# Performance work log

Measured on AMD Instinct MI355X. Metric: run time of the kernel, lower is better.

## Reference

```python
import jax, jax.numpy as jnp
import numpy as np

BATCH = 16384
MAX_ACTIVE = 32
FEAT = 768
HIDDEN = 1024


def setup_inputs() -> dict:
    key = jax.random.key(0)
    k1, k2, k3, k4, k5, k6 = jax.random.split(key, 6)
    stm = jax.random.randint(k1, (BATCH, MAX_ACTIVE), 0, FEAT, dtype=jnp.int32)
    nstm = jax.random.randint(k2, (BATCH, MAX_ACTIVE), 0, FEAT, dtype=jnp.int32)
    # Linear params (PyTorch layout: weight is (out_features, in_features))
    ft_w = jax.random.normal(k3, (HIDDEN, FEAT), dtype=jnp.float32) * 0.05
    ft_b = jax.random.normal(k4, (HIDDEN,), dtype=jnp.float32) * 0.05
    out_w = jax.random.normal(k5, (1, 2 * HIDDEN), dtype=jnp.float32) * 0.05
    out_b = jax.random.normal(k6, (1,), dtype=jnp.float32) * 0.05
    return {"stm": stm, "nstm": nstm, "ft_w": ft_w, "ft_b": ft_b,
            "out_w": out_w, "out_b": out_b}


def sparse_to_dense(indices: jnp.ndarray, size: int = FEAT) -> jnp.ndarray:
    """(B, max_active) int indices with -1 padding -> (B, size) 0/1 float32."""
    b = indices.shape[0]
    valid = (indices >= 0).astype(jnp.float32)          # (B, A)
    cols = jnp.clip(indices, 0, size - 1)               # padded -> col 0, masked by `valid`
    rows = jnp.arange(b, dtype=jnp.int32)[:, None]      # (B, 1) broadcast
    dense = jnp.zeros((b, size), dtype=jnp.float32)
    # .max matches torch's set-to-1 semantics even if duplicate indices occur
    return dense.at[rows, cols].max(valid)


def reference(stm, nstm, ft_w, ft_b, out_w, out_b):
    stm_d = sparse_to_dense(stm)                        # (B, 768)
    nstm_d = sparse_to_dense(nstm)                      # (B, 768)
    stm_h = stm_d @ ft_w.T + ft_b                       # (B, H)
    nstm_h = nstm_d @ ft_w.T + ft_b                     # (B, H)
    hidden = jnp.concatenate([stm_h, nstm_h], axis=1)   # (B, 2H)
    hidden = jnp.clip(hidden, 0.0, 1.0)
    return jax.nn.sigmoid(hidden @ out_w.T + out_b)     # (B, 1)
```

## Files before the change

### kernel.cpp

```cpp
#include <hip/hip_runtime.h>
#include <stdint.h>

#define BATCH 16384
#define MAXA 32
#define FEAT 768
#define HIDDEN 1024

#define KC 24
#define NT 32
#define ASTRIDE 784
#define AWBYTES (32 * ASTRIDE)
#define BTILE (KC * 1024)

typedef int v4i  __attribute__((ext_vector_type(4)));
typedef int v16i __attribute__((ext_vector_type(16)));

__global__ __launch_bounds__(256) void prep_quant(const float* __restrict__ ftw,
                                                  uint8_t* __restrict__ Bf,
                                                  float* __restrict__ scale,
                                                  float* __restrict__ outz) {
  const int h0 = blockIdx.x * 8;
  const int hloc = threadIdx.x >> 5;
  const int l32 = threadIdx.x & 31;
  const int h = h0 + hloc;

  float w[24];
  float amax = 0.f;
  const float* __restrict__ src = ftw + (size_t)h * FEAT;
#pragma unroll
  for (int k = 0; k < 24; ++k) {
    w[k] = src[l32 + 32 * k];
    amax = fmaxf(amax, fabsf(w[k]));
  }
#pragma unroll
  for (int m = 1; m <= 16; m <<= 1)
    amax = fmaxf(amax, __shfl_xor(amax, m, 64));
  amax = fmaxf(amax, 1e-20f);
  if (l32 == 0) scale[h] = amax / 127.f;
  const float inv = 127.f / amax;

  __shared__ __align__(16) uint8_t tile[8][ASTRIDE];
#pragma unroll
  for (int k = 0; k < 24; ++k) {
    int q = __float2int_rn(w[k] * inv);
    tile[hloc][l32 + 32 * k] = (uint8_t)(int8_t)q;
  }
  __syncthreads();

  for (int g = threadIdx.x; g < 8 * 48; g += 256) {
    int hl = g / 48, fg = g % 48;
    int kc = fg >> 1, lh = fg & 1;
    int hh = h0 + hl;
    uint4 v = *(const uint4*)&tile[hl][fg * 16];
    size_t daddr = ((size_t)((hh >> 5) * KC + kc) << 10) +
                   (size_t)(((lh << 5) | (hh & 31)) << 4);
    *(uint4*)(Bf + daddr) = v;
  }

  if (threadIdx.x < 128)
    outz[blockIdx.x * 128 + threadIdx.x] = 0.f;
}

__global__ __launch_bounds__(256, 1) void nn_mfma(
    const int* __restrict__ stm, const int* __restrict__ nstm,
    const uint8_t* __restrict__ Bf, const float* __restrict__ scale,
    const float* __restrict__ bias, const float* __restrict__ outw,
    float* __restrict__ outz)
{
  const int tid  = threadIdx.x;
  const int lane = tid & 63;
  const int wid  = tid >> 6;
  const int side = wid & 1;
  const int rgrp = wid >> 1;
  const int r0   = blockIdx.x * 64 + rgrp * 32;
  const int l31  = lane & 31;
  const int lh   = lane >> 5;

  __shared__ __align__(16) uint8_t Ash[4 * AWBYTES];
  __shared__ __align__(16) uint8_t Bbuf[2][BTILE];

  uint8_t* Aw = Ash + wid * AWBYTES;

  uint4 st[6];
  {
    const uint4* g = (const uint4*)Bf;
#pragma unroll
    for (int s = 0; s < 6; ++s) st[s] = g[s * 256 + tid];
  }

  const uint4 z4 = {0u, 0u, 0u, 0u};
#pragma unroll
  for (int it = 0; it < 25; ++it) {
    int off = it * 1024 + lane * 16;
    if (off < AWBYTES) *(uint4*)(Aw + off) = z4;
  }
  const int* __restrict__ isrc = side ? nstm : stm;
#pragma unroll
  for (int i = 0; i < 16; ++i) {
    int row = i * 2 + lh;
    int idx = isrc[(r0 + row) * MAXA + l31];
    if (idx >= 0) Aw[row * ASTRIDE + idx] = 1;
  }
  v4i areg[KC];
#pragma unroll
  for (int kc = 0; kc < KC; ++kc)
    areg[kc] = *(const v4i*)(Aw + l31 * ASTRIDE + kc * 32 + lh * 16);

#pragma unroll
  for (int s = 0; s < 6; ++s) ((uint4*)Bbuf[0])[s * 256 + tid] = st[s];
  __syncthreads();

  float* sbo = (float*)Ash;
  {
    const float4* gs = (const float4*)scale;
    const float4* gb = (const float4*)bias;
    const float4* go = (const float4*)outw;
    float4* d = (float4*)sbo;
    d[tid]       = gs[tid];
    d[256 + tid] = gb[tid];
    d[512 + tid] = go[tid];
    d[768 + tid] = go[256 + tid];
  }
  __syncthreads();

  float prow[16];
#pragma unroll
  for (int r = 0; r < 16; ++r) prow[r] = 0.f;

#pragma unroll 1
  for (int nt = 0; nt < NT; ++nt) {
    const int p = nt & 1;
    if (nt + 1 < NT) {
      const uint4* g = (const uint4*)(Bf + (size_t)(nt + 1) * BTILE);
#pragma unroll
      for (int s = 0; s < 6; ++s) st[s] = g[s * 256 + tid];
    }
    v16i acc;
#pragma unroll
    for (int r = 0; r < 16; ++r) acc[r] = 0;
    const uint8_t* bp = Bbuf[p];
#pragma unroll
    for (int kc = 0; kc < KC; ++kc) {
      v4i b = *(const v4i*)(bp + kc * 1024 + lane * 16);
      acc = __builtin_amdgcn_mfma_i32_32x32x32_i8(areg[kc], b, acc, 0, 0, 0);
    }
    float s  = sbo[nt * 32 + l31];
    float bb = sbo[1024 + nt * 32 + l31];
    float o  = sbo[2048 + side * HIDDEN + nt * 32 + l31];
#pragma unroll
    for (int r = 0; r < 16; ++r) {
      float hv = fminf(fmaxf(fmaf((float)acc[r], s, bb), 0.f), 1.f);
      prow[r] = fmaf(hv, o, prow[r]);
    }
    if (nt + 1 < NT) {
      uint4* d = (uint4*)Bbuf[p ^ 1];
#pragma unroll
      for (int s2 = 0; s2 < 6; ++s2) d[s2 * 256 + tid] = st[s2];
    }
    __syncthreads();
  }

#pragma unroll
  for (int off = 16; off >= 1; off >>= 1)
#pragma unroll
    for (int r = 0; r < 16; ++r) prow[r] += __shfl_xor(prow[r], off, 64);

  if (l31 == 0) {
#pragma unroll
    for (int r = 0; r < 16; ++r) {
      int row = (r & 3) + 8 * (r >> 2) + 4 * lh;
      atomicAdd(&outz[r0 + row], prow[r]);
    }
  }
}

__global__ __launch_bounds__(256) void nn_finish(float* __restrict__ outz,
                                                 const float* __restrict__ outb) {
  const int i = blockIdx.x * 256 + threadIdx.x;
  float y = outz[i] + outb[0];
  outz[i] = 1.f / (1.f + __expf(-y));
}

extern "C" void kernel_launch(void* const* d_in, const int* in_sizes, int n_in,
                              void* d_out, int out_size, void* d_ws, size_t ws_size,
                              hipStream_t stream) {
  const int*   stm  = (const int*)d_in[0];
  const int*   nstm = (const int*)d_in[1];
  const float* ftw  = (const float*)d_in[2];
  const float* ftb  = (const float*)d_in[3];
  const float* outw = (const float*)d_in[4];
  const float* outb = (const float*)d_in[5];

  uint8_t* Bf    = (uint8_t*)d_ws;
  float*   scale = (float*)(Bf + (size_t)FEAT * HIDDEN);
  float*   outz  = (float*)d_out;

  prep_quant<<<HIDDEN / 8, 256, 0, stream>>>(ftw, Bf, scale, outz);
  nn_mfma<<<BATCH / 64, 256, 0, stream>>>(stm, nstm, Bf, scale, ftb, outw, outz);
  nn_finish<<<BATCH / 256, 256, 0, stream>>>(outz, outb);
}
```

Measured before the change: 140.8 us.

## Process two row tiles per wave and split hidden dimension across block pairs

Each block now handles 128 batch rows instead of 64, with every wave holding two 32-row A fragments in registers, and the hidden dimension is split in half across paired blocks. Each B tile loaded into LDS therefore feeds two MFMAs, which halves B traffic per row computed while keeping the grid size the same. Register pressure roughly doubles for the A operands and accumulators, which could cause spills, and the number of atomics per output row doubles.

```diff
diff --git a/kernel.cpp b/kernel.cpp
--- a/kernel.cpp
+++ b/kernel.cpp
@@ -7,7 +7,7 @@
 #define HIDDEN 1024
 
 #define KC 24
-#define NT 32
+#define NTH 16
 #define ASTRIDE 784
 #define AWBYTES (32 * ASTRIDE)
 #define BTILE (KC * 1024)
@@ -72,7 +72,8 @@
   const int wid  = tid >> 6;
   const int side = wid & 1;
   const int rgrp = wid >> 1;
-  const int r0   = blockIdx.x * 64 + rgrp * 32;
+  const int nh   = blockIdx.x & 1;
+  const int R    = (blockIdx.x >> 1) * 128;
   const int l31  = lane & 31;
   const int lh   = lane >> 5;
 
@@ -83,28 +84,31 @@
 
   uint4 st[6];
   {
-    const uint4* g = (const uint4*)Bf;
+    const uint4* g = (const uint4*)(Bf + (size_t)(nh * NTH) * BTILE);
 #pragma unroll
     for (int s = 0; s < 6; ++s) st[s] = g[s * 256 + tid];
   }
 
+  const int* __restrict__ isrc = side ? nstm : stm;
   const uint4 z4 = {0u, 0u, 0u, 0u};
-#pragma unroll
-  for (int it = 0; it < 25; ++it) {
-    int off = it * 1024 + lane * 16;
-    if (off < AWBYTES) *(uint4*)(Aw + off) = z4;
-  }
-  const int* __restrict__ isrc = side ? nstm : stm;
-#pragma unroll
-  for (int i = 0; i < 16; ++i) {
-    int row = i * 2 + lh;
-    int idx = isrc[(r0 + row) * MAXA + l31];
-    if (idx >= 0) Aw[row * ASTRIDE + idx] = 1;
-  }
-  v4i areg[KC];
-#pragma unroll
-  for (int kc = 0; kc < KC; ++kc)
-    areg[kc] = *(const v4i*)(Aw + l31 * ASTRIDE + kc * 32 + lh * 16);
+  v4i areg[2][KC];
+#pragma unroll
+  for (int t = 0; t < 2; ++t) {
+#pragma unroll
+    for (int it = 0; it < 25; ++it) {
+      int off = it * 1024 + lane * 16;
+      if (off < AWBYTES) *(uint4*)(Aw + off) = z4;
+    }
+#pragma unroll
+    for (int i = 0; i < 16; ++i) {
+      int row = i * 2 + lh;
+      int idx = isrc[(R + rgrp * 64 + t * 32 + row) * MAXA + l31];
+      if (idx >= 0) Aw[row * ASTRIDE + idx] = 1;
+    }
+#pragma unroll
+    for (int kc = 0; kc < KC; ++kc)
+      areg[t][kc] = *(const v4i*)(Aw + l31 * ASTRIDE + kc * 32 + lh * 16);
+  }
 
 #pragma unroll
   for (int s = 0; s < 6; ++s) ((uint4*)Bbuf[0])[s * 256 + tid] = st[s];
@@ -112,47 +116,49 @@
 
   float* sbo = (float*)Ash;
   {
-    const float4* gs = (const float4*)scale;
-    const float4* gb = (const float4*)bias;
-    const float4* go = (const float4*)outw;
+    const float4* g0 = (const float4*)(scale + nh * 512);
+    const float4* g1 = (const float4*)(bias + nh * 512);
+    const float4* g2 = (const float4*)(outw + nh * 512);
+    const float4* g3 = (const float4*)(outw + HIDDEN + nh * 512);
     float4* d = (float4*)sbo;
-    d[tid]       = gs[tid];
-    d[256 + tid] = gb[tid];
-    d[512 + tid] = go[tid];
-    d[768 + tid] = go[256 + tid];
+    d[tid]       = (tid < 128) ? g0[tid] : g1[tid - 128];
+    d[256 + tid] = (tid < 128) ? g2[tid] : g3[tid - 128];
   }
   __syncthreads();
 
-  float prow[16];
-#pragma unroll
-  for (int r = 0; r < 16; ++r) prow[r] = 0.f;
+  float prow0[16], prow1[16];
+#pragma unroll
+  for (int r = 0; r < 16; ++r) { prow0[r] = 0.f; prow1[r] = 0.f; }
 
 #pragma unroll 1
-  for (int nt = 0; nt < NT; ++nt) {
+  for (int nt = 0; nt < NTH; ++nt) {
     const int p = nt & 1;
-    if (nt + 1 < NT) {
-      const uint4* g = (const uint4*)(Bf + (size_t)(nt + 1) * BTILE);
+    if (nt + 1 < NTH) {
+      const uint4* g = (const uint4*)(Bf + (size_t)(nh * NTH + nt + 1) * BTILE);
 #pragma unroll
       for (int s = 0; s < 6; ++s) st[s] = g[s * 256 + tid];
     }
-    v16i acc;
-#pragma unroll
-    for (int r = 0; r < 16; ++r) acc[r] = 0;
+    v16i acc0, acc1;
+#pragma unroll
+    for (int r = 0; r < 16; ++r) { acc0[r] = 0; acc1[r] = 0; }
     const uint8_t* bp = Bbuf[p];
 #pragma unroll
     for (int kc = 0; kc < KC; ++kc) {
       v4i b = *(const v4i*)(bp + kc * 1024 + lane * 16);
-      acc = __builtin_amdgcn_mfma_i32_32x32x32_i8(areg[kc], b, acc, 0, 0, 0);
+      acc0 = __builtin_amdgcn_mfma_i32_32x32x32_i8(areg[0][kc], b, acc0, 0, 0, 0);
+      acc1 = __builtin_amdgcn_mfma_i32_32x32x32_i8(areg[1][kc], b, acc1, 0, 0, 0);
     }
     float s  = sbo[nt * 32 + l31];
-    float bb = sbo[1024 + nt * 32 + l31];
-    float o  = sbo[2048 + side * HIDDEN + nt * 32 + l31];
+    float bb = sbo[512 + nt * 32 + l31];
+    float o  = sbo[1024 + side * 512 + nt * 32 + l31];
 #pragma unroll
     for (int r = 0; r < 16; ++r) {
-      float hv = fminf(fmaxf(fmaf((float)acc[r], s, bb), 0.f), 1.f);
-      prow[r] = fmaf(hv, o, prow[r]);
-    }
-    if (nt + 1 < NT) {
+      float h0 = fminf(fmaxf(fmaf((float)acc0[r], s, bb), 0.f), 1.f);
+      float h1 = fminf(fmaxf(fmaf((float)acc1[r], s, bb), 0.f), 1.f);
+      prow0[r] = fmaf(h0, o, prow0[r]);
+      prow1[r] = fmaf(h1, o, prow1[r]);
+    }
+    if (nt + 1 < NTH) {
       uint4* d = (uint4*)Bbuf[p ^ 1];
 #pragma unroll
       for (int s2 = 0; s2 < 6; ++s2) d[s2 * 256 + tid] = st[s2];
@@ -163,13 +169,17 @@
 #pragma unroll
   for (int off = 16; off >= 1; off >>= 1)
 #pragma unroll
-    for (int r = 0; r < 16; ++r) prow[r] += __shfl_xor(prow[r], off, 64);
+    for (int r = 0; r < 16; ++r) {
+      prow0[r] += __shfl_xor(prow0[r], off, 64);
+      prow1[r] += __shfl_xor(prow1[r], off, 64);
+    }
 
   if (l31 == 0) {
 #pragma unroll
     for (int r = 0; r < 16; ++r) {
-      int row = (r & 3) + 8 * (r >> 2) + 4 * lh;
-      atomicAdd(&outz[r0 + row], prow[r]);
+      int crow = (r & 3) + 8 * (r >> 2) + 4 * lh;
+      atomicAdd(&outz[R + rgrp * 64 + crow], prow0[r]);
+      atomicAdd(&outz[R + rgrp * 64 + 32 + crow], prow1[r]);
     }
   }
 }
@@ -196,6 +206,7 @@
   float*   outz  = (float*)d_out;
 
   prep_quant<<<HIDDEN / 8, 256, 0, stream>>>(ftw, Bf, scale, outz);
-  nn_mfma<<<BATCH / 64, 256, 0, stream>>>(stm, nstm, Bf, scale, ftb, outw, outz);
+  nn_mfma<<<(BATCH / 128) * 2, 256, 0, stream>>>(stm, nstm, Bf, scale, ftb,
+                                                 outw, outz);
   nn_finish<<<BATCH / 256, 256, 0, stream>>>(outz, outb);
 }
```

New measurement: 138.6 us. No clear change (-1.5%).

## Split hidden dim across blocks, bitmap A build, stream B directly from global

Applied to the files above, without the earlier changes.

Each block now takes 128 rows and one half of the hidden dimension (512 threads, 8 waves), so the grid doubles and each wave runs 16 N-tiles instead of 32. The dense one-hot A tile is replaced by a 32-bit-per-word bitmap in LDS built with atomicOr, then expanded to int8 bytes in registers by a multiply-and-mask trick. This shrinks LDS use enough for 2 blocks per CU. The LDS double-buffering of B is removed: waves read B fragments straight from global/L2, which drops all per-tile barriers. Two independent accumulators let consecutive MFMAs run without waiting on each other. The risk is heavier global/L2 traffic for B, since each wave re-reads it with no shared staging.

```diff
diff --git a/kernel.cpp b/kernel.cpp
--- a/kernel.cpp
+++ b/kernel.cpp
@@ -7,10 +7,9 @@
 #define HIDDEN 1024
 
 #define KC 24
-#define NT 32
+#define NTH 16
+#define BTILE (KC * 1024)
 #define ASTRIDE 784
-#define AWBYTES (32 * ASTRIDE)
-#define BTILE (KC * 1024)
 
 typedef int v4i  __attribute__((ext_vector_type(4)));
 typedef int v16i __attribute__((ext_vector_type(16)));
@@ -61,7 +60,7 @@
     outz[blockIdx.x * 128 + threadIdx.x] = 0.f;
 }
 
-__global__ __launch_bounds__(256, 1) void nn_mfma(
+__global__ __launch_bounds__(512, 2) void nn_mfma(
     const int* __restrict__ stm, const int* __restrict__ nstm,
     const uint8_t* __restrict__ Bf, const float* __restrict__ scale,
     const float* __restrict__ bias, const float* __restrict__ outw,
@@ -72,92 +71,79 @@
   const int wid  = tid >> 6;
   const int side = wid & 1;
   const int rgrp = wid >> 1;
-  const int r0   = blockIdx.x * 64 + rgrp * 32;
+  const int nh   = blockIdx.x & 1;
+  const int R    = (blockIdx.x >> 1) * 128;
   const int l31  = lane & 31;
   const int lh   = lane >> 5;
 
-  __shared__ __align__(16) uint8_t Ash[4 * AWBYTES];
-  __shared__ __align__(16) uint8_t Bbuf[2][BTILE];
+  __shared__ uint32_t amap[8][32 * 24];
+  __shared__ float    sbo[2048];
 
-  uint8_t* Aw = Ash + wid * AWBYTES;
-
-  uint4 st[6];
   {
-    const uint4* g = (const uint4*)Bf;
-#pragma unroll
-    for (int s = 0; s < 6; ++s) st[s] = g[s * 256 + tid];
+    float4* d = (float4*)sbo;
+    if (tid < 128)       d[tid] = ((const float4*)(scale + nh * 512))[tid];
+    else if (tid < 256)  d[tid] = ((const float4*)(bias + nh * 512))[tid - 128];
+    else if (tid < 384)  d[tid] = ((const float4*)(outw + nh * 512))[tid - 256];
+    else                 d[tid] = ((const float4*)(outw + HIDDEN + nh * 512))[tid - 384];
   }
 
-  const uint4 z4 = {0u, 0u, 0u, 0u};
-#pragma unroll
-  for (int it = 0; it < 25; ++it) {
-    int off = it * 1024 + lane * 16;
-    if (off < AWBYTES) *(uint4*)(Aw + off) = z4;
+  uint32_t* mp = amap[wid];
+  {
+    const uint4 z = {0u, 0u, 0u, 0u};
+    ((uint4*)mp)[lane] = z;
+    ((uint4*)mp)[64 + lane] = z;
+    ((uint4*)mp)[128 + lane] = z;
   }
   const int* __restrict__ isrc = side ? nstm : stm;
 #pragma unroll
   for (int i = 0; i < 16; ++i) {
-    int row = i * 2 + lh;
-    int idx = isrc[(r0 + row) * MAXA + l31];
-    if (idx >= 0) Aw[row * ASTRIDE + idx] = 1;
+    int row = 2 * i + lh;
+    int idx = isrc[(R + rgrp * 32 + row) * MAXA + l31];
+    if (idx >= 0) atomicOr(&mp[row * 24 + (idx >> 5)], 1u << (idx & 31));
   }
+  __syncthreads();
+
   v4i areg[KC];
 #pragma unroll
-  for (int kc = 0; kc < KC; ++kc)
-    areg[kc] = *(const v4i*)(Aw + l31 * ASTRIDE + kc * 32 + lh * 16);
-
+  for (int kc = 0; kc < KC; ++kc) {
+    uint32_t wbits = mp[l31 * 24 + kc];
+    uint32_t hbits = (wbits >> (lh * 16)) & 0xFFFFu;
+    v4i a;
 #pragma unroll
-  for (int s = 0; s < 6; ++s) ((uint4*)Bbuf[0])[s * 256 + tid] = st[s];
-  __syncthreads();
-
-  float* sbo = (float*)Ash;
-  {
-    const float4* gs = (const float4*)scale;
-    const float4* gb = (const float4*)bias;
-    const float4* go = (const float4*)outw;
-    float4* d = (float4*)sbo;
-    d[tid]       = gs[tid];
-    d[256 + tid] = gb[tid];
-    d[512 + tid] = go[tid];
-    d[768 + tid] = go[256 + tid];
+    for (int j = 0; j < 4; ++j)
+      a[j] = (int)((((hbits >> (4 * j)) & 0xFu) * 0x00204081u) & 0x01010101u);
+    areg[kc] = a;
   }
-  __syncthreads();
 
   float prow[16];
 #pragma unroll
   for (int r = 0; r < 16; ++r) prow[r] = 0.f;
 
+  const uint8_t* __restrict__ Bbase =
+      Bf + (size_t)(nh * NTH) * BTILE + (size_t)lane * 16;
+
 #pragma unroll 1
-  for (int nt = 0; nt < NT; ++nt) {
-    const int p = nt & 1;
-    if (nt + 1 < NT) {
-      const uint4* g = (const uint4*)(Bf + (size_t)(nt + 1) * BTILE);
+  for (int nt = 0; nt < NTH; ++nt) {
+    const uint8_t* bp = Bbase + (size_t)nt * BTILE;
+    v16i acc0, acc1;
 #pragma unroll
-      for (int s = 0; s < 6; ++s) st[s] = g[s * 256 + tid];
-    }
-    v16i acc;
+    for (int r = 0; r < 16; ++r) { acc0[r] = 0; acc1[r] = 0; }
 #pragma unroll
-    for (int r = 0; r < 16; ++r) acc[r] = 0;
-    const uint8_t* bp = Bbuf[p];
-#pragma unroll
-    for (int kc = 0; kc < KC; ++kc) {
-      v4i b = *(const v4i*)(bp + kc * 1024 + lane * 16);
-      acc = __builtin_amdgcn_mfma_i32_32x32x32_i8(areg[kc], b, acc, 0, 0, 0);
+    for (int kc = 0; kc < KC; kc += 2) {
+      v4i b0 = *(const v4i*)(bp + (size_t)kc * 1024);
+      v4i b1 = *(const v4i*)(bp + (size_t)kc * 1024 + 1024);
+      acc0 = __builtin_amdgcn_mfma_i32_32x32x32_i8(areg[kc], b0, acc0, 0, 0, 0);
+      acc1 = __builtin_amdgcn_mfma_i32_32x32x32_i8(areg[kc + 1], b1, acc1, 0, 0, 0);
     }
     float s  = sbo[nt * 32 + l31];
-    float bb = sbo[1024 + nt * 32 + l31];
-    float o  = sbo[2048 + side * HIDDEN + nt * 32 + l31];
+    float bb = sbo[512 + nt * 32 + l31];
+    float o  = sbo[1024 + side * 512 + nt * 32 + l31];
 #pragma unroll
     for (int r = 0; r < 16; ++r) {
-      float hv = fminf(fmaxf(fmaf((float)acc[r], s, bb), 0.f), 1.f);
+      int q = acc0[r] + acc1[r];
+      float hv = fminf(fmaxf(fmaf((float)q, s, bb), 0.f), 1.f);
       prow[r] = fmaf(hv, o, prow[r]);
     }
-    if (nt + 1 < NT) {
-      uint4* d = (uint4*)Bbuf[p ^ 1];
-#pragma unroll
-      for (int s2 = 0; s2 < 6; ++s2) d[s2 * 256 + tid] = st[s2];
-    }
-    __syncthreads();
   }
 
 #pragma unroll
@@ -168,8 +154,8 @@
   if (l31 == 0) {
 #pragma unroll
     for (int r = 0; r < 16; ++r) {
-      int row = (r & 3) + 8 * (r >> 2) + 4 * lh;
-      atomicAdd(&outz[r0 + row], prow[r]);
+      int crow = (r & 3) + 8 * (r >> 2) + 4 * lh;
+      atomicAdd(&outz[R + rgrp * 32 + crow], prow[r]);
     }
   }
 }
@@ -196,6 +182,7 @@
   float*   outz  = (float*)d_out;
 
   prep_quant<<<HIDDEN / 8, 256, 0, stream>>>(ftw, Bf, scale, outz);
-  nn_mfma<<<BATCH / 64, 256, 0, stream>>>(stm, nstm, Bf, scale, ftb, outw, outz);
+  nn_mfma<<<(BATCH / 128) * 2, 512, 0, stream>>>(stm, nstm, Bf, scale, ftb,
+                                                 outw, outz);
   nn_finish<<<BATCH / 256, 256, 0, stream>>>(outz, outb);
 }
```

Result: slower. 170.5 us (+21.1%).
